# Kernel tuning notes

Hardware: AMD Instinct MI355X
Metric: run time of the kernel (lower is better)

Reference implementation:

```python
import jax, jax.numpy as jnp
import numpy as np

N = 50000

def sage_conv(x, src, dst, W_l, b_l, W_r):
    # mean aggregation of source-node features onto destination nodes
    msgs = x[src]                                   # [E, F] gather
    agg = jax.ops.segment_sum(msgs, dst, num_segments=N)  # [N, F]
    ones = jnp.ones((src.shape[0],), dtype=x.dtype)
    deg = jax.ops.segment_sum(ones, dst, num_segments=N)  # [N]
    agg = agg / jnp.maximum(deg, 1.0)[:, None]
    # out = lin_l(agg) + lin_r(x); lin_l has bias, lin_r does not (PyG default)
    return agg @ W_l.T + b_l + x @ W_r.T


def setup_inputs() -> dict:
    key = jax.random.key(0)
    ks = jax.random.split(key, 8)
    dim_in, dim_h, dim_out = 128, 128, 64
    E = 640000
    x = jax.random.normal(ks[0], (N, dim_in), dtype=jnp.float32)
    edge_index = jax.random.randint(ks[1], (2, E), 0, N, dtype=jnp.int64)
    s = 1.0 / np.sqrt(dim_in)
    W1_l = jax.random.uniform(ks[2], (dim_h, dim_in), minval=-s, maxval=s, dtype=jnp.float32)
    b1 = jnp.zeros((dim_h,), dtype=jnp.float32)
    W1_r = jax.random.uniform(ks[3], (dim_h, dim_in), minval=-s, maxval=s, dtype=jnp.float32)
    s2 = 1.0 / np.sqrt(dim_h)
    W2_l = jax.random.uniform(ks[4], (dim_out, dim_h), minval=-s2, maxval=s2, dtype=jnp.float32)
    b2 = jnp.zeros((dim_out,), dtype=jnp.float32)
    W2_r = jax.random.uniform(ks[5], (dim_out, dim_h), minval=-s2, maxval=s2, dtype=jnp.float32)
    return {"x": x, "edge_index": edge_index, "W1_l": W1_l, "b1": b1, "W1_r": W1_r,
            "W2_l": W2_l, "b2": b2, "W2_r": W2_r}


def reference(x, edge_index, W1_l, b1, W1_r, W2_l, b2, W2_r):
    src, dst = edge_index[0], edge_index[1]
    h = sage_conv(x, src, dst, W1_l, b1, W1_r)
    h = jax.nn.relu(h)
    # dropout(p=0.5) is identity in eval mode
    h = sage_conv(h, src, dst, W2_l, b2, W2_r)
    return jax.nn.log_softmax(h, axis=1)
```

## Files before the change

### kernel.cpp

```cpp
#include <hip/hip_runtime.h>

#define N_NODES 50000
#define TILES (N_NODES / 16)
#define NB 196
#define BSHIFT 8
#define CAP 4096
#define CONV_BLOCKS 3125

typedef __bf16 v8bf __attribute__((ext_vector_type(8)));
typedef float v4f __attribute__((ext_vector_type(4)));

union ABfrag { uint4 u; v8bf v; };

__device__ __forceinline__ float bf2f(unsigned short u) {
    union { unsigned int i; float f; } c; c.i = ((unsigned int)u) << 16; return c.f;
}
__device__ __forceinline__ unsigned short f2bf(float f) {
    union { float f; unsigned int i; } c; c.f = f;
    unsigned int r = c.i + 0x7FFFu + ((c.i >> 16) & 1u);
    return (unsigned short)(r >> 16);
}
__device__ __forceinline__ void acc8(float* a, uint4 u) {
    a[0] += bf2f((unsigned short)u.x); a[1] += bf2f((unsigned short)(u.x >> 16));
    a[2] += bf2f((unsigned short)u.y); a[3] += bf2f((unsigned short)(u.y >> 16));
    a[4] += bf2f((unsigned short)u.z); a[5] += bf2f((unsigned short)(u.z >> 16));
    a[6] += bf2f((unsigned short)u.w); a[7] += bf2f((unsigned short)(u.w >> 16));
}

__global__ __launch_bounds__(256) void setup_conv_kernel(
    const float* __restrict__ x, unsigned short* __restrict__ xbf,
    const float* __restrict__ W1l, const float* __restrict__ W1r,
    const float* __restrict__ W2l, const float* __restrict__ W2r,
    unsigned short* __restrict__ Wp1, unsigned short* __restrict__ Wp2l,
    unsigned short* __restrict__ Wp2r, int* __restrict__ gcur)
{
    int t = threadIdx.x;
    if (blockIdx.x < CONV_BLOCKS) {
        int i = blockIdx.x * 256 + t;
        const float4* p = reinterpret_cast<const float4*>(x) + (size_t)i * 2;
        float4 a = p[0], b = p[1];
        uint4 o;
        o.x = (unsigned int)f2bf(a.x) | ((unsigned int)f2bf(a.y) << 16);
        o.y = (unsigned int)f2bf(a.z) | ((unsigned int)f2bf(a.w) << 16);
        o.z = (unsigned int)f2bf(b.x) | ((unsigned int)f2bf(b.y) << 16);
        o.w = (unsigned int)f2bf(b.z) | ((unsigned int)f2bf(b.w) << 16);
        reinterpret_cast<uint4*>(xbf)[i] = o;
        return;
    }
    int gid = (blockIdx.x - CONV_BLOCKS) * 256 + t;
    if (gid < 32768) {
        int p = gid;
        int i = p & 7, lane = (p >> 3) & 63, q = p >> 9;
        int nf = q % 8, ks = q / 8;
        int k = ks * 32 + 4 * (lane >> 4) + (i & 3) + 16 * (i >> 2);
        int n = nf * 16 + (lane & 15);
        float w = (k < 128) ? W1l[n * 128 + k] : W1r[n * 128 + (k - 128)];
        Wp1[p] = f2bf(w);
    } else if (gid < 40960) {
        int p = gid - 32768;
        int i = p & 7, lane = (p >> 3) & 63, q = p >> 9;
        int nf = q % 4, ks = q / 4;
        int k = ks * 32 + 4 * (lane >> 4) + (i & 3) + 16 * (i >> 2);
        int n = nf * 16 + (lane & 15);
        Wp2l[p] = f2bf(W2l[n * 128 + k]);
    } else if (gid < 49152) {
        int p = gid - 40960;
        int i = p & 7, lane = (p >> 3) & 63, q = p >> 9;
        int nf = q % 4, ks = q / 4;
        int k = ks * 32 + 4 * (lane >> 4) + (i & 3) + 16 * (i >> 2);
        int n = nf * 16 + (lane & 15);
        Wp2r[p] = f2bf(W2r[n * 128 + k]);
    } else if (gid < 49152 + NB) {
        gcur[gid - 49152] = (gid - 49152) * CAP;
    }
}

__global__ __launch_bounds__(256) void bucketFill_kernel(
    const int* __restrict__ ei, int* __restrict__ gcur,
    unsigned int* __restrict__ arena, int E)
{
    __shared__ int h[NB];
    __shared__ int base[NB];
    int t = threadIdx.x;
    if (t < NB) h[t] = 0;
    __syncthreads();
    int i = blockIdx.x * 256 + t;
    bool act = (i * 4 < E);
    int4 s4, d4;
    if (act) {
        s4 = reinterpret_cast<const int4*>(ei)[i];
        d4 = reinterpret_cast<const int4*>(ei + E)[i];
        atomicAdd(&h[d4.x >> BSHIFT], 1);
        atomicAdd(&h[d4.y >> BSHIFT], 1);
        atomicAdd(&h[d4.z >> BSHIFT], 1);
        atomicAdd(&h[d4.w >> BSHIFT], 1);
    }
    __syncthreads();
    if (t < NB) {
        int c = h[t];
        base[t] = c ? atomicAdd(&gcur[t], c) : 0;
        h[t] = 0;
    }
    __syncthreads();
    if (act) {
        int b; unsigned p;
        b = d4.x >> BSHIFT; p = base[b] + atomicAdd(&h[b], 1);
        arena[p] = (unsigned)s4.x | ((unsigned)(d4.x & 255) << 16);
        b = d4.y >> BSHIFT; p = base[b] + atomicAdd(&h[b], 1);
        arena[p] = (unsigned)s4.y | ((unsigned)(d4.y & 255) << 16);
        b = d4.z >> BSHIFT; p = base[b] + atomicAdd(&h[b], 1);
        arena[p] = (unsigned)s4.z | ((unsigned)(d4.z & 255) << 16);
        b = d4.w >> BSHIFT; p = base[b] + atomicAdd(&h[b], 1);
        arena[p] = (unsigned)s4.w | ((unsigned)(d4.w & 255) << 16);
    }
}

__global__ __launch_bounds__(256) void bucketCSR_kernel(
    const unsigned int* __restrict__ arena, const int* __restrict__ gcur,
    int* __restrict__ row_start, int* __restrict__ row_end,
    int* __restrict__ col)
{
    __shared__ int cnt[256];
    __shared__ int s[256];
    __shared__ int cur[256];
    int b = blockIdx.x, t = threadIdx.x;
    int es = b * CAP, ee = gcur[b];
    cnt[t] = 0;
    __syncthreads();
    for (int j = es + t; j < ee; j += 256)
        atomicAdd(&cnt[arena[j] >> 16], 1);
    __syncthreads();
    int v = cnt[t];
    s[t] = v;
    __syncthreads();
#pragma unroll
    for (int off = 1; off < 256; off <<= 1) {
        int u = (t >= off) ? s[t - off] : 0;
        __syncthreads();
        s[t] += u;
        __syncthreads();
    }
    int end = es + s[t];
    int node = (b << BSHIFT) + t;
    if (node < N_NODES) {
        row_start[node] = end - v;
        row_end[node]   = end;
    }
    cur[t] = end - v;
    __syncthreads();
    for (int j = es + t; j < ee; j += 256) {
        unsigned e = arena[j];
        int pos = atomicAdd(&cur[e >> 16], 1);
        col[pos] = (int)(e & 0xFFFFu);
    }
}

__global__ __launch_bounds__(256) void gather_mean_bf16_kernel(
    const unsigned short* __restrict__ feat,
    const int* __restrict__ row_start,
    const int* __restrict__ row_end,
    const int* __restrict__ col,
    unsigned short* __restrict__ aggm,
    int nNodes)
{
    int node = blockIdx.x * 16 + (threadIdx.x >> 4);
    if (node >= nNodes) return;
    int c = threadIdx.x & 15;
    int rs = row_start[node], re = row_end[node];
    const uint4* f4 = reinterpret_cast<const uint4*>(feat);

    float a[8] = {0.f, 0.f, 0.f, 0.f, 0.f, 0.f, 0.f, 0.f};
    float b[8] = {0.f, 0.f, 0.f, 0.f, 0.f, 0.f, 0.f, 0.f};
    int j = rs;
    for (; j + 7 < re; j += 8) {
        int cc[8];
#pragma unroll
        for (int q = 0; q < 8; ++q) cc[q] = col[j + q];
        uint4 u[8];
#pragma unroll
        for (int q = 0; q < 8; ++q) u[q] = f4[(size_t)cc[q] * 16 + c];
#pragma unroll
        for (int q = 0; q < 8; ++q) acc8((q & 1) ? b : a, u[q]);
    }
    for (; j + 3 < re; j += 4) {
        int c0 = col[j], c1 = col[j + 1], c2 = col[j + 2], c3 = col[j + 3];
        uint4 u0 = f4[(size_t)c0 * 16 + c];
        uint4 u1 = f4[(size_t)c1 * 16 + c];
        uint4 u2 = f4[(size_t)c2 * 16 + c];
        uint4 u3 = f4[(size_t)c3 * 16 + c];
        acc8(a, u0); acc8(b, u1); acc8(a, u2); acc8(b, u3);
    }
    for (; j < re; ++j) acc8(a, f4[(size_t)col[j] * 16 + c]);

    float inv = 1.0f / fmaxf((float)(re - rs), 1.0f);
    uint4 o;
    o.x = (unsigned int)f2bf((a[0] + b[0]) * inv) | ((unsigned int)f2bf((a[1] + b[1]) * inv) << 16);
    o.y = (unsigned int)f2bf((a[2] + b[2]) * inv) | ((unsigned int)f2bf((a[3] + b[3]) * inv) << 16);
    o.z = (unsigned int)f2bf((a[4] + b[4]) * inv) | ((unsigned int)f2bf((a[5] + b[5]) * inv) << 16);
    o.w = (unsigned int)f2bf((a[6] + b[6]) * inv) | ((unsigned int)f2bf((a[7] + b[7]) * inv) << 16);
    reinterpret_cast<uint4*>(aggm)[(size_t)node * 16 + c] = o;
}

__global__ __launch_bounds__(256) void dense1_mfma_kernel(
    const unsigned short* __restrict__ aggm,
    const unsigned short* __restrict__ xbf,
    const unsigned short* __restrict__ Wp,
    const unsigned short* __restrict__ Wp2l,
    const unsigned short* __restrict__ Wp2r,
    const float* __restrict__ bias,
    const float* __restrict__ bias2,
    unsigned short* __restrict__ p2,
    unsigned short* __restrict__ q2)
{
    __shared__ unsigned short A[2 * 16 * 136];
    const int t = threadIdx.x;
    const int w = t >> 6;
    const int lane = t & 63;
    const int m = lane & 15;
    const int g = lane >> 4;

    ABfrag wf[2][8];
    ABfrag wf2l[4], wf2r[4];
    const uint4* wp4 = reinterpret_cast<const uint4*>(Wp);
    const uint4* wpl = reinterpret_cast<const uint4*>(Wp2l);
    const uint4* wpr = reinterpret_cast<const uint4*>(Wp2r);
#pragma unroll
    for (int ks = 0; ks < 8; ++ks)
#pragma unroll
        for (int nf = 0; nf < 2; ++nf)
            wf[nf][ks].u = wp4[(size_t)(ks * 8 + (w * 2 + nf)) * 64 + lane];
#pragma unroll
    for (int ks = 0; ks < 4; ++ks) {
        wf2l[ks].u = wpl[(size_t)(ks * 4 + w) * 64 + lane];
        wf2r[ks].u = wpr[(size_t)(ks * 4 + w) * 64 + lane];
    }

    float bv0 = bias[w * 32 + m];
    float bv1 = bias[w * 32 + 16 + m];
    float bv2 = bias2[w * 16 + m];

    for (int tile = blockIdx.x; tile < TILES; tile += gridDim.x) {
        int nb0 = tile * 16;
        {
            int row = t >> 4, c = t & 15;
            uint4 v0 = reinterpret_cast<const uint4*>(aggm)[(size_t)(nb0 + row) * 16 + c];
            uint4 v1 = reinterpret_cast<const uint4*>(xbf )[(size_t)(nb0 + row) * 16 + c];
            *reinterpret_cast<uint4*>(&A[row * 136 + c * 8]) = v0;
            *reinterpret_cast<uint4*>(&A[2176 + row * 136 + c * 8]) = v1;
        }
        __syncthreads();

        v4f acc0 = {bv0, bv0, bv0, bv0};
        v4f acc1 = {bv1, bv1, bv1, bv1};
#pragma unroll
        for (int ks = 0; ks < 8; ++ks) {
            int half = ks >> 2, ksl = ks & 3;
            const unsigned short* base = &A[half * 2176 + m * 136 + ksl * 32 + 4 * g];
            uint2 lo = *reinterpret_cast<const uint2*>(base);
            uint2 hi = *reinterpret_cast<const uint2*>(base + 16);
            ABfrag af; af.u = make_uint4(lo.x, lo.y, hi.x, hi.y);
            acc0 = __builtin_amdgcn_mfma_f32_16x16x32_bf16(af.v, wf[0][ks].v, acc0, 0, 0, 0);
            acc1 = __builtin_amdgcn_mfma_f32_16x16x32_bf16(af.v, wf[1][ks].v, acc1, 0, 0, 0);
        }
        __syncthreads();

#pragma unroll
        for (int r = 0; r < 4; ++r) {
            A[(4 * g + r) * 136 + w * 32 + m]      = f2bf(fmaxf(acc0[r], 0.f));
            A[(4 * g + r) * 136 + w * 32 + 16 + m] = f2bf(fmaxf(acc1[r], 0.f));
        }
        __syncthreads();

        v4f accp = {0.f, 0.f, 0.f, 0.f};
        v4f accq = {bv2, bv2, bv2, bv2};
#pragma unroll
        for (int ks = 0; ks < 4; ++ks) {
            const unsigned short* base = &A[m * 136 + ks * 32 + 4 * g];
            uint2 lo = *reinterpret_cast<const uint2*>(base);
            uint2 hi = *reinterpret_cast<const uint2*>(base + 16);
            ABfrag af; af.u = make_uint4(lo.x, lo.y, hi.x, hi.y);
            accp = __builtin_amdgcn_mfma_f32_16x16x32_bf16(af.v, wf2l[ks].v, accp, 0, 0, 0);
            accq = __builtin_amdgcn_mfma_f32_16x16x32_bf16(af.v, wf2r[ks].v, accq, 0, 0, 0);
        }
#pragma unroll
        for (int r = 0; r < 4; ++r) {
            A[2176 + (4 * g + r) * 136 + w * 16 + m]      = f2bf(accp[r]);
            A[2176 + (4 * g + r) * 136 + 64 + w * 16 + m] = f2bf(accq[r]);
        }
        __syncthreads();
        {
            int tt = t & 127;
            int row = tt >> 3, c = tt & 7;
            if (t < 128) {
                uint4 v = *reinterpret_cast<const uint4*>(&A[2176 + row * 136 + c * 8]);
                reinterpret_cast<uint4*>(p2)[(size_t)(nb0 + row) * 8 + c] = v;
            } else {
                uint4 v = *reinterpret_cast<const uint4*>(&A[2176 + row * 136 + 64 + c * 8]);
                reinterpret_cast<uint4*>(q2)[(size_t)(nb0 + row) * 8 + c] = v;
            }
        }
        __syncthreads();
    }
}

__global__ __launch_bounds__(256) void out_kernel(
    const unsigned short* __restrict__ p2,
    const unsigned short* __restrict__ q2,
    const int* __restrict__ row_start,
    const int* __restrict__ row_end,
    const int* __restrict__ col,
    float* __restrict__ out,
    int nNodes)
{
    int node = blockIdx.x * 32 + (threadIdx.x >> 3);
    if (node >= nNodes) return;
    int c = threadIdx.x & 7;
    int rs = row_start[node], re = row_end[node];
    const uint4* f4 = reinterpret_cast<const uint4*>(p2);

    float a[8] = {0.f, 0.f, 0.f, 0.f, 0.f, 0.f, 0.f, 0.f};
    float b[8] = {0.f, 0.f, 0.f, 0.f, 0.f, 0.f, 0.f, 0.f};
    int j = rs;
    for (; j + 7 < re; j += 8) {
        int cc[8];
#pragma unroll
        for (int q = 0; q < 8; ++q) cc[q] = col[j + q];
        uint4 u[8];
#pragma unroll
        for (int q = 0; q < 8; ++q) u[q] = f4[(size_t)cc[q] * 8 + c];
#pragma unroll
        for (int q = 0; q < 8; ++q) acc8((q & 1) ? b : a, u[q]);
    }
    for (; j + 3 < re; j += 4) {
        int c0 = col[j], c1 = col[j + 1], c2 = col[j + 2], c3 = col[j + 3];
        uint4 u0 = f4[(size_t)c0 * 8 + c];
        uint4 u1 = f4[(size_t)c1 * 8 + c];
        uint4 u2 = f4[(size_t)c2 * 8 + c];
        uint4 u3 = f4[(size_t)c3 * 8 + c];
        acc8(a, u0); acc8(b, u1); acc8(a, u2); acc8(b, u3);
    }
    for (; j < re; ++j) acc8(a, f4[(size_t)col[j] * 8 + c]);

    float inv = 1.0f / fmaxf((float)(re - rs), 1.0f);
    uint4 qv = reinterpret_cast<const uint4*>(q2)[(size_t)node * 8 + c];
    float v[8];
    v[0] = (a[0] + b[0]) * inv + bf2f((unsigned short)qv.x);
    v[1] = (a[1] + b[1]) * inv + bf2f((unsigned short)(qv.x >> 16));
    v[2] = (a[2] + b[2]) * inv + bf2f((unsigned short)qv.y);
    v[3] = (a[3] + b[3]) * inv + bf2f((unsigned short)(qv.y >> 16));
    v[4] = (a[4] + b[4]) * inv + bf2f((unsigned short)qv.z);
    v[5] = (a[5] + b[5]) * inv + bf2f((unsigned short)(qv.z >> 16));
    v[6] = (a[6] + b[6]) * inv + bf2f((unsigned short)qv.w);
    v[7] = (a[7] + b[7]) * inv + bf2f((unsigned short)(qv.w >> 16));

    float mx = v[0];
#pragma unroll
    for (int q = 1; q < 8; ++q) mx = fmaxf(mx, v[q]);
#pragma unroll
    for (int s = 1; s < 8; s <<= 1) mx = fmaxf(mx, __shfl_xor(mx, s, 8));
    float sum = 0.f;
#pragma unroll
    for (int q = 0; q < 8; ++q) sum += expf(v[q] - mx);
#pragma unroll
    for (int s = 1; s < 8; s <<= 1) sum += __shfl_xor(sum, s, 8);
    float lse = mx + logf(sum);

    float4 o0 = {v[0] - lse, v[1] - lse, v[2] - lse, v[3] - lse};
    float4 o1 = {v[4] - lse, v[5] - lse, v[6] - lse, v[7] - lse};
    float4* op = reinterpret_cast<float4*>(out + (size_t)node * 64);
    op[c * 2]     = o0;
    op[c * 2 + 1] = o1;
}

extern "C" void kernel_launch(void* const* d_in, const int* in_sizes, int n_in,
                              void* d_out, int out_size, void* d_ws, size_t ws_size,
                              hipStream_t stream)
{
    const float* x   = (const float*)d_in[0];
    const int*   ei  = (const int*)d_in[1];
    const float* W1l = (const float*)d_in[2];
    const float* b1  = (const float*)d_in[3];
    const float* W1r = (const float*)d_in[4];
    const float* W2l = (const float*)d_in[5];
    const float* b2  = (const float*)d_in[6];
    const float* W2r = (const float*)d_in[7];
    float* out = (float*)d_out;

    const int E = in_sizes[1] / 2;

    int* gcur      = (int*)d_ws;
    int* row_start = gcur + NB;
    int* row_end   = row_start + N_NODES;
    int* col       = row_end + N_NODES;
    unsigned int* arena = (unsigned int*)(col + NB * CAP);
    size_t off_i = (size_t)NB + 2 * (size_t)N_NODES + 2 * (size_t)(NB * CAP);
    off_i = (off_i + 3) & ~(size_t)3;
    unsigned short* xbf   = (unsigned short*)((int*)d_ws + off_i);
    unsigned short* aggm  = xbf  + (size_t)N_NODES * 128;
    unsigned short* p2    = aggm + (size_t)N_NODES * 128;
    unsigned short* q2    = p2   + (size_t)N_NODES * 64;
    unsigned short* Wp1   = q2   + (size_t)N_NODES * 64;
    unsigned short* Wp2l  = Wp1 + 32768;
    unsigned short* Wp2r  = Wp2l + 8192;

    const int eb4 = (E / 4 + 255) / 256;

    setup_conv_kernel<<<CONV_BLOCKS + 193, 256, 0, stream>>>(
        x, xbf, W1l, W1r, W2l, W2r, Wp1, Wp2l, Wp2r, gcur);
    bucketFill_kernel<<<eb4, 256, 0, stream>>>(ei, gcur, arena, E);
    bucketCSR_kernel<<<NB, 256, 0, stream>>>(arena, gcur, row_start, row_end, col);

    gather_mean_bf16_kernel<<<(N_NODES + 15) / 16, 256, 0, stream>>>(
        xbf, row_start, row_end, col, aggm, N_NODES);
    dense1_mfma_kernel<<<1024, 256, 0, stream>>>(
        aggm, xbf, Wp1, Wp2l, Wp2r, b1, b2, p2, q2);

    out_kernel<<<(N_NODES + 31) / 32, 256, 0, stream>>>(
        p2, q2, row_start, row_end, col, out, N_NODES);
}
```

Before: 105.8 us.

## Fuse layer-1 neighbor mean gather into the dense MFMA kernel

The separate gather-mean kernel is merged into the dense layer kernel. Each block now gathers and averages neighbor features for its 16-node tile straight into shared memory, then runs both MFMA layers. This removes the bf16 aggm round trip through global memory and one launch. In exchange, the grid becomes one block per tile (3125) instead of a persistent 1024-block loop, so weight fragments are reloaded per tile and the gather's latency is no longer hidden behind other kernels' work.

```diff
diff --git a/kernel.cpp b/kernel.cpp
--- a/kernel.cpp
+++ b/kernel.cpp
@@ -155,55 +155,11 @@
     }
 }
 
-__global__ __launch_bounds__(256) void gather_mean_bf16_kernel(
-    const unsigned short* __restrict__ feat,
+__global__ __launch_bounds__(256) void dense1_fused_kernel(
+    const unsigned short* __restrict__ xbf,
     const int* __restrict__ row_start,
     const int* __restrict__ row_end,
     const int* __restrict__ col,
-    unsigned short* __restrict__ aggm,
-    int nNodes)
-{
-    int node = blockIdx.x * 16 + (threadIdx.x >> 4);
-    if (node >= nNodes) return;
-    int c = threadIdx.x & 15;
-    int rs = row_start[node], re = row_end[node];
-    const uint4* f4 = reinterpret_cast<const uint4*>(feat);
-
-    float a[8] = {0.f, 0.f, 0.f, 0.f, 0.f, 0.f, 0.f, 0.f};
-    float b[8] = {0.f, 0.f, 0.f, 0.f, 0.f, 0.f, 0.f, 0.f};
-    int j = rs;
-    for (; j + 7 < re; j += 8) {
-        int cc[8];
-#pragma unroll
-        for (int q = 0; q < 8; ++q) cc[q] = col[j + q];
-        uint4 u[8];
-#pragma unroll
-        for (int q = 0; q < 8; ++q) u[q] = f4[(size_t)cc[q] * 16 + c];
-#pragma unroll
-        for (int q = 0; q < 8; ++q) acc8((q & 1) ? b : a, u[q]);
-    }
-    for (; j + 3 < re; j += 4) {
-        int c0 = col[j], c1 = col[j + 1], c2 = col[j + 2], c3 = col[j + 3];
-        uint4 u0 = f4[(size_t)c0 * 16 + c];
-        uint4 u1 = f4[(size_t)c1 * 16 + c];
-        uint4 u2 = f4[(size_t)c2 * 16 + c];
-        uint4 u3 = f4[(size_t)c3 * 16 + c];
-        acc8(a, u0); acc8(b, u1); acc8(a, u2); acc8(b, u3);
-    }
-    for (; j < re; ++j) acc8(a, f4[(size_t)col[j] * 16 + c]);
-
-    float inv = 1.0f / fmaxf((float)(re - rs), 1.0f);
-    uint4 o;
-    o.x = (unsigned int)f2bf((a[0] + b[0]) * inv) | ((unsigned int)f2bf((a[1] + b[1]) * inv) << 16);
-    o.y = (unsigned int)f2bf((a[2] + b[2]) * inv) | ((unsigned int)f2bf((a[3] + b[3]) * inv) << 16);
-    o.z = (unsigned int)f2bf((a[4] + b[4]) * inv) | ((unsigned int)f2bf((a[5] + b[5]) * inv) << 16);
-    o.w = (unsigned int)f2bf((a[6] + b[6]) * inv) | ((unsigned int)f2bf((a[7] + b[7]) * inv) << 16);
-    reinterpret_cast<uint4*>(aggm)[(size_t)node * 16 + c] = o;
-}
-
-__global__ __launch_bounds__(256) void dense1_mfma_kernel(
-    const unsigned short* __restrict__ aggm,
-    const unsigned short* __restrict__ xbf,
     const unsigned short* __restrict__ Wp,
     const unsigned short* __restrict__ Wp2l,
     const unsigned short* __restrict__ Wp2r,
@@ -218,6 +174,50 @@
     const int lane = t & 63;
     const int m = lane & 15;
     const int g = lane >> 4;
+    const int nb0 = blockIdx.x * 16;
+
+    {
+        int row = t >> 4, c = t & 15;
+        uint4 v1 = reinterpret_cast<const uint4*>(xbf)[(size_t)(nb0 + row) * 16 + c];
+        *reinterpret_cast<uint4*>(&A[2176 + row * 136 + c * 8]) = v1;
+    }
+    {
+        int nl = t >> 4, cl = t & 15;
+        int node = nb0 + nl;
+        int rs = row_start[node], re = row_end[node];
+        const uint4* f4 = reinterpret_cast<const uint4*>(xbf);
+        float a[8] = {0.f, 0.f, 0.f, 0.f, 0.f, 0.f, 0.f, 0.f};
+        float b[8] = {0.f, 0.f, 0.f, 0.f, 0.f, 0.f, 0.f, 0.f};
+        int j = rs;
+        for (; j + 7 < re; j += 8) {
+            int cc[8];
+#pragma unroll
+            for (int q = 0; q < 8; ++q) cc[q] = col[j + q];
+            uint4 u[8];
+#pragma unroll
+            for (int q = 0; q < 8; ++q) u[q] = f4[(size_t)cc[q] * 16 + cl];
+#pragma unroll
+            for (int q = 0; q < 8; ++q) acc8((q & 1) ? b : a, u[q]);
+        }
+        for (; j + 3 < re; j += 4) {
+            int c0 = col[j], c1 = col[j + 1], c2 = col[j + 2], c3 = col[j + 3];
+            uint4 u0 = f4[(size_t)c0 * 16 + cl];
+            uint4 u1 = f4[(size_t)c1 * 16 + cl];
+            uint4 u2 = f4[(size_t)c2 * 16 + cl];
+            uint4 u3 = f4[(size_t)c3 * 16 + cl];
+            acc8(a, u0); acc8(b, u1); acc8(a, u2); acc8(b, u3);
+        }
+        for (; j < re; ++j) acc8(a, f4[(size_t)col[j] * 16 + cl]);
+
+        float inv = 1.0f / fmaxf((float)(re - rs), 1.0f);
+        uint4 o;
+        o.x = (unsigned int)f2bf((a[0] + b[0]) * inv) | ((unsigned int)f2bf((a[1] + b[1]) * inv) << 16);
+        o.y = (unsigned int)f2bf((a[2] + b[2]) * inv) | ((unsigned int)f2bf((a[3] + b[3]) * inv) << 16);
+        o.z = (unsigned int)f2bf((a[4] + b[4]) * inv) | ((unsigned int)f2bf((a[5] + b[5]) * inv) << 16);
+        o.w = (unsigned int)f2bf((a[6] + b[6]) * inv) | ((unsigned int)f2bf((a[7] + b[7]) * inv) << 16);
+        *reinterpret_cast<uint4*>(&A[nl * 136 + cl * 8]) = o;
+    }
+    __syncthreads();
 
     ABfrag wf[2][8];
     ABfrag wf2l[4], wf2r[4];
@@ -234,72 +234,58 @@
         wf2l[ks].u = wpl[(size_t)(ks * 4 + w) * 64 + lane];
         wf2r[ks].u = wpr[(size_t)(ks * 4 + w) * 64 + lane];
     }
-
     float bv0 = bias[w * 32 + m];
     float bv1 = bias[w * 32 + 16 + m];
     float bv2 = bias2[w * 16 + m];
 
-    for (int tile = blockIdx.x; tile < TILES; tile += gridDim.x) {
-        int nb0 = tile * 16;
-        {
-            int row = t >> 4, c = t & 15;
-            uint4 v0 = reinterpret_cast<const uint4*>(aggm)[(size_t)(nb0 + row) * 16 + c];
-            uint4 v1 = reinterpret_cast<const uint4*>(xbf )[(size_t)(nb0 + row) * 16 + c];
-            *reinterpret_cast<uint4*>(&A[row * 136 + c * 8]) = v0;
-            *reinterpret_cast<uint4*>(&A[2176 + row * 136 + c * 8]) = v1;
+    v4f acc0 = {bv0, bv0, bv0, bv0};
+    v4f acc1 = {bv1, bv1, bv1, bv1};
+#pragma unroll
+    for (int ks = 0; ks < 8; ++ks) {
+        int half = ks >> 2, ksl = ks & 3;
+        const unsigned short* base = &A[half * 2176 + m * 136 + ksl * 32 + 4 * g];
+        uint2 lo = *reinterpret_cast<const uint2*>(base);
+        uint2 hi = *reinterpret_cast<const uint2*>(base + 16);
+        ABfrag af; af.u = make_uint4(lo.x, lo.y, hi.x, hi.y);
+        acc0 = __builtin_amdgcn_mfma_f32_16x16x32_bf16(af.v, wf[0][ks].v, acc0, 0, 0, 0);
+        acc1 = __builtin_amdgcn_mfma_f32_16x16x32_bf16(af.v, wf[1][ks].v, acc1, 0, 0, 0);
+    }
+    __syncthreads();
+
+#pragma unroll
+    for (int r = 0; r < 4; ++r) {
+        A[(4 * g + r) * 136 + w * 32 + m]      = f2bf(fmaxf(acc0[r], 0.f));
+        A[(4 * g + r) * 136 + w * 32 + 16 + m] = f2bf(fmaxf(acc1[r], 0.f));
+    }
+    __syncthreads();
+
+    v4f accp = {0.f, 0.f, 0.f, 0.f};
+    v4f accq = {bv2, bv2, bv2, bv2};
+#pragma unroll
+    for (int ks = 0; ks < 4; ++ks) {
+        const unsigned short* base = &A[m * 136 + ks * 32 + 4 * g];
+        uint2 lo = *reinterpret_cast<const uint2*>(base);
+        uint2 hi = *reinterpret_cast<const uint2*>(base + 16);
+        ABfrag af; af.u = make_uint4(lo.x, lo.y, hi.x, hi.y);
+        accp = __builtin_amdgcn_mfma_f32_16x16x32_bf16(af.v, wf2l[ks].v, accp, 0, 0, 0);
+        accq = __builtin_amdgcn_mfma_f32_16x16x32_bf16(af.v, wf2r[ks].v, accq, 0, 0, 0);
+    }
+#pragma unroll
+    for (int r = 0; r < 4; ++r) {
+        A[2176 + (4 * g + r) * 136 + w * 16 + m]      = f2bf(accp[r]);
+        A[2176 + (4 * g + r) * 136 + 64 + w * 16 + m] = f2bf(accq[r]);
+    }
+    __syncthreads();
+    {
+        int tt = t & 127;
+        int row = tt >> 3, c = tt & 7;
+        if (t < 128) {
+            uint4 v = *reinterpret_cast<const uint4*>(&A[2176 + row * 136 + c * 8]);
+            reinterpret_cast<uint4*>(p2)[(size_t)(nb0 + row) * 8 + c] = v;
+        } else {
+            uint4 v = *reinterpret_cast<const uint4*>(&A[2176 + row * 136 + 64 + c * 8]);
+            reinterpret_cast<uint4*>(q2)[(size_t)(nb0 + row) * 8 + c] = v;
         }
-        __syncthreads();
-
-        v4f acc0 = {bv0, bv0, bv0, bv0};
-        v4f acc1 = {bv1, bv1, bv1, bv1};
-#pragma unroll
-        for (int ks = 0; ks < 8; ++ks) {
-            int half = ks >> 2, ksl = ks & 3;
-            const unsigned short* base = &A[half * 2176 + m * 136 + ksl * 32 + 4 * g];
-            uint2 lo = *reinterpret_cast<const uint2*>(base);
-            uint2 hi = *reinterpret_cast<const uint2*>(base + 16);
-            ABfrag af; af.u = make_uint4(lo.x, lo.y, hi.x, hi.y);
-            acc0 = __builtin_amdgcn_mfma_f32_16x16x32_bf16(af.v, wf[0][ks].v, acc0, 0, 0, 0);
-            acc1 = __builtin_amdgcn_mfma_f32_16x16x32_bf16(af.v, wf[1][ks].v, acc1, 0, 0, 0);
-        }
-        __syncthreads();
-
-#pragma unroll
-        for (int r = 0; r < 4; ++r) {
-            A[(4 * g + r) * 136 + w * 32 + m]      = f2bf(fmaxf(acc0[r], 0.f));
-            A[(4 * g + r) * 136 + w * 32 + 16 + m] = f2bf(fmaxf(acc1[r], 0.f));
-        }
-        __syncthreads();
-
-        v4f accp = {0.f, 0.f, 0.f, 0.f};
-        v4f accq = {bv2, bv2, bv2, bv2};
-#pragma unroll
-        for (int ks = 0; ks < 4; ++ks) {
-            const unsigned short* base = &A[m * 136 + ks * 32 + 4 * g];
-            uint2 lo = *reinterpret_cast<const uint2*>(base);
-            uint2 hi = *reinterpret_cast<const uint2*>(base + 16);
-            ABfrag af; af.u = make_uint4(lo.x, lo.y, hi.x, hi.y);
-            accp = __builtin_amdgcn_mfma_f32_16x16x32_bf16(af.v, wf2l[ks].v, accp, 0, 0, 0);
-            accq = __builtin_amdgcn_mfma_f32_16x16x32_bf16(af.v, wf2r[ks].v, accq, 0, 0, 0);
-        }
-#pragma unroll
-        for (int r = 0; r < 4; ++r) {
-            A[2176 + (4 * g + r) * 136 + w * 16 + m]      = f2bf(accp[r]);
-            A[2176 + (4 * g + r) * 136 + 64 + w * 16 + m] = f2bf(accq[r]);
-        }
-        __syncthreads();
-        {
-            int tt = t & 127;
-            int row = tt >> 3, c = tt & 7;
-            if (t < 128) {
-                uint4 v = *reinterpret_cast<const uint4*>(&A[2176 + row * 136 + c * 8]);
-                reinterpret_cast<uint4*>(p2)[(size_t)(nb0 + row) * 8 + c] = v;
-            } else {
-                uint4 v = *reinterpret_cast<const uint4*>(&A[2176 + row * 136 + 64 + c * 8]);
-                reinterpret_cast<uint4*>(q2)[(size_t)(nb0 + row) * 8 + c] = v;
-            }
-        }
-        __syncthreads();
     }
 }
 
@@ -396,10 +382,9 @@
     size_t off_i = (size_t)NB + 2 * (size_t)N_NODES + 2 * (size_t)(NB * CAP);
     off_i = (off_i + 3) & ~(size_t)3;
     unsigned short* xbf   = (unsigned short*)((int*)d_ws + off_i);
-    unsigned short* aggm  = xbf  + (size_t)N_NODES * 128;
-    unsigned short* p2    = aggm + (size_t)N_NODES * 128;
-    unsigned short* q2    = p2   + (size_t)N_NODES * 64;
-    unsigned short* Wp1   = q2   + (size_t)N_NODES * 64;
+    unsigned short* p2    = xbf + (size_t)N_NODES * 128;
+    unsigned short* q2    = p2  + (size_t)N_NODES * 64;
+    unsigned short* Wp1   = q2  + (size_t)N_NODES * 64;
     unsigned short* Wp2l  = Wp1 + 32768;
     unsigned short* Wp2r  = Wp2l + 8192;
 
@@ -410,10 +395,8 @@
     bucketFill_kernel<<<eb4, 256, 0, stream>>>(ei, gcur, arena, E);
     bucketCSR_kernel<<<NB, 256, 0, stream>>>(arena, gcur, row_start, row_end, col);
 
-    gather_mean_bf16_kernel<<<(N_NODES + 15) / 16, 256, 0, stream>>>(
-        xbf, row_start, row_end, col, aggm, N_NODES);
-    dense1_mfma_kernel<<<1024, 256, 0, stream>>>(
-        aggm, xbf, Wp1, Wp2l, Wp2r, b1, b2, p2, q2);
+    dense1_fused_kernel<<<TILES, 256, 0, stream>>>(
+        xbf, row_start, row_end, col, Wp1, Wp2l, Wp2r, b1, b2, p2, q2);
 
     out_kernel<<<(N_NODES + 31) / 32, 256, 0, stream>>>(
         p2, q2, row_start, row_end, col, out, N_NODES);
```

New measurement: 103.0 us. 1.03x faster.
